# Kernel tuning notes

Measured on AMD Instinct MI355X. Metric: run time of the kernel, lower is better.

Reference implementation:

```python
import jax
import jax.numpy as jnp
import numpy as np

B, S, D, H, HID, E, TOPK = 1, 2048, 1024, 16, 4096, 8, 2
HEAD_DIM = D // H


def _layer_norm(x, g, b, eps=1e-5):
    mu = jnp.mean(x, axis=-1, keepdims=True)
    var = jnp.var(x, axis=-1, keepdims=True)
    return (x - mu) * jax.lax.rsqrt(var + eps) * g + b


def setup_inputs() -> dict:
    key = jax.random.key(0)
    ks = jax.random.split(key, 12)
    s = 0.02
    return {
        "x": jax.random.normal(ks[0], (B, S, D), jnp.float32),
        "ln1_g": jnp.ones((D,), jnp.float32),
        "ln1_b": jnp.zeros((D,), jnp.float32),
        "wq": jax.random.normal(ks[1], (D, D), jnp.float32) * s,
        "wk": jax.random.normal(ks[2], (D, D), jnp.float32) * s,
        "wv": jax.random.normal(ks[3], (D, D), jnp.float32) * s,
        "wo": jax.random.normal(ks[4], (D, D), jnp.float32) * s,
        "ln2_g": jnp.ones((D,), jnp.float32),
        "ln2_b": jnp.zeros((D,), jnp.float32),
        "w_gate": jax.random.normal(ks[5], (D, E), jnp.float32) * s,
        "w_eg": jax.random.normal(ks[6], (E, D, HID), jnp.float32) * s,
        "w_eu": jax.random.normal(ks[7], (E, D, HID), jnp.float32) * s,
        "w_ed": jax.random.normal(ks[8], (E, HID, D), jnp.float32) * s,
    }


def _attention(h, wq, wk, wv, wo):
    b, s, d = h.shape
    q = (h @ wq).reshape(b, s, H, HEAD_DIM).transpose(0, 2, 1, 3)
    k = (h @ wk).reshape(b, s, H, HEAD_DIM).transpose(0, 2, 1, 3)
    v = (h @ wv).reshape(b, s, H, HEAD_DIM).transpose(0, 2, 1, 3)
    scores = jnp.einsum("bhqd,bhkd->bhqk", q, k) / jnp.sqrt(jnp.asarray(HEAD_DIM, h.dtype))
    causal = jnp.tril(jnp.ones((s, s), bool))  # [s,s]
    scores = jnp.where(causal, scores, jnp.asarray(-1e30, h.dtype))
    attn = jax.nn.softmax(scores, axis=-1)
    out = jnp.einsum("bhqk,bhkd->bhqd", attn, v).transpose(0, 2, 1, 3).reshape(b, s, d)
    return out @ wo


def _moe(h, w_gate, w_eg, w_eu, w_ed):
    b, s, d = h.shape
    flat = h.reshape(-1, d)  # [T,D]
    logits = flat @ w_gate  # [T,E]
    scores = jax.nn.sigmoid(logits)
    top_val, top_idx = jax.lax.top_k(scores, TOPK)
    top_val = top_val / (jnp.sum(top_val, axis=-1, keepdims=True) + 1e-9)
    # per-token per-expert combine weight (0 for unrouted experts)
    combine = jnp.sum(jax.nn.one_hot(top_idx, E, dtype=flat.dtype) * top_val[..., None], axis=1)  # [T,E]
    g = jax.nn.silu(jnp.einsum("td,edh->eth", flat, w_eg))
    u = jnp.einsum("td,edh->eth", flat, w_eu)
    eo = jnp.einsum("eth,ehd->etd", g * u, w_ed)  # [E,T,D]
    out = jnp.einsum("etd,te->td", eo, combine)
    return out.reshape(b, s, d)


def reference(x, ln1_g, ln1_b, wq, wk, wv, wo, ln2_g, ln2_b, w_gate, w_eg, w_eu, w_ed):
    x = x + _attention(_layer_norm(x, ln1_g, ln1_b), wq, wk, wv, wo)
    x = x + _moe(_layer_norm(x, ln2_g, ln2_b), w_gate, w_eg, w_eu, w_ed)
    return x
```

## Files before the change

### kernel.cpp

```cpp
#include <hip/hip_runtime.h>
#include <hip/hip_bf16.h>
#include <stdint.h>

#define DI __device__ __forceinline__

typedef short bf16x8_t __attribute__((ext_vector_type(8)));
typedef float f32x4_t __attribute__((ext_vector_type(4)));

DI unsigned short f2bf(float f) {
  __hip_bfloat16 h = __float2bfloat16(f);
  unsigned short u;
  __builtin_memcpy(&u, &h, 2);
  return u;
}

DI uint32_t pk2(float a, float b) {
  return (uint32_t)f2bf(a) | ((uint32_t)f2bf(b) << 16);
}

DI f32x4_t mfma16(bf16x8_t a, bf16x8_t b, f32x4_t c) {
  return __builtin_amdgcn_mfma_f32_16x16x32_bf16(a, b, c, 0, 0, 0);
}

DI void gload16(const void* g, void* l) {
  __builtin_amdgcn_global_load_lds(
      (const __attribute__((address_space(1))) uint32_t*)g,
      (__attribute__((address_space(3))) uint32_t*)l, 16, 0, 0);
}

DI bf16x8_t frag(const unsigned short* base, int row, int hi) {
  return *(const bf16x8_t*)&base[row * 32 + ((hi ^ ((row >> 1) & 3)) * 8)];
}
DI int chunk_swz(int tid) { return ((tid & 3) ^ ((tid >> 3) & 3)) * 8; }

__global__ __launch_bounds__(256) void transpose_cvt(const float* __restrict__ in,
                                                     unsigned short* __restrict__ out,
                                                     int R, int C) {
  __shared__ float tile[64][65];
  const int tid = threadIdx.x;
  const int tx = tid & 15, ty = tid >> 4;
  const size_t zoff = (size_t)blockIdx.z * R * C;
  const int r0 = blockIdx.y * 64, c0 = blockIdx.x * 64;
#pragma unroll
  for (int i = 0; i < 4; ++i) {
    const int r = ty + i * 16;
    const float4 v = *(const float4*)(in + zoff + (size_t)(r0 + r) * C + c0 + tx * 4);
    tile[r][tx * 4 + 0] = v.x; tile[r][tx * 4 + 1] = v.y;
    tile[r][tx * 4 + 2] = v.z; tile[r][tx * 4 + 3] = v.w;
  }
  __syncthreads();
#pragma unroll
  for (int i = 0; i < 4; ++i) {
    const int r = ty + i * 16;
    ushort4 o;
    o.x = f2bf(tile[tx * 4 + 0][r]); o.y = f2bf(tile[tx * 4 + 1][r]);
    o.z = f2bf(tile[tx * 4 + 2][r]); o.w = f2bf(tile[tx * 4 + 3][r]);
    *(ushort4*)(out + zoff + (size_t)(c0 + r) * R + r0 + tx * 4) = o;
  }
}

__global__ __launch_bounds__(256) void ln_kernel(const float* __restrict__ x, const float* __restrict__ g,
                                                 const float* __restrict__ b, unsigned short* __restrict__ out) {
  const int row = blockIdx.x, tid = threadIdx.x;
  const int wid = tid >> 6, lane = tid & 63;
  const float4 v = *(const float4*)(x + (size_t)row * 1024 + tid * 4);
  float s = v.x + v.y + v.z + v.w;
  float s2 = v.x * v.x + v.y * v.y + v.z * v.z + v.w * v.w;
#pragma unroll
  for (int o = 1; o < 64; o <<= 1) { s += __shfl_xor(s, o); s2 += __shfl_xor(s2, o); }
  __shared__ float red[8];
  if (lane == 0) { red[wid] = s; red[4 + wid] = s2; }
  __syncthreads();
  const float ts = red[0] + red[1] + red[2] + red[3];
  const float ts2 = red[4] + red[5] + red[6] + red[7];
  const float mu = ts * 0.0009765625f;
  const float var = ts2 * 0.0009765625f - mu * mu;
  const float rs = rsqrtf(var + 1e-5f);
  const float4 gg = *(const float4*)(g + tid * 4);
  const float4 bb = *(const float4*)(b + tid * 4);
  ushort4 o4;
  o4.x = f2bf((v.x - mu) * rs * gg.x + bb.x);
  o4.y = f2bf((v.y - mu) * rs * gg.y + bb.y);
  o4.z = f2bf((v.z - mu) * rs * gg.z + bb.z);
  o4.w = f2bf((v.w - mu) * rs * gg.w + bb.w);
  *(ushort4*)(out + (size_t)row * 1024 + tid * 4) = o4;
}

template<int BN>
DI void gemm_loop(const unsigned short* aR0, const unsigned short* aR1,
                  const unsigned short* bR0, const unsigned short* bR1,
                  const int K, unsigned short* lds, const int tid,
                  f32x4_t (&acc)[4][BN / 32]) {
  constexpr int NF = BN / 32;
  unsigned short* ldsA = lds;
  unsigned short* ldsB = lds + 4096;
  const int wid = tid >> 6, lane = tid & 63, ln = lane & 15, hi = lane >> 4;
  const int wr = wid >> 1, wc = wid & 1;
  char* dstA0 = (char*)ldsA + wid * 1024;
  char* dstA1 = (char*)ldsA + 4096 + wid * 1024;
  char* dstB0 = (char*)ldsB + wid * 1024;
  char* dstB1 = (char*)ldsB + 4096 + wid * 1024;
  for (int k0 = 0; k0 < K; k0 += 32) {
    gload16(aR0 + k0, dstA0);
    gload16(aR1 + k0, dstA1);
    gload16(bR0 + k0, dstB0);
    if constexpr (BN == 128) gload16(bR1 + k0, dstB1);
    __syncthreads();
    bf16x8_t af[4];
#pragma unroll
    for (int mf = 0; mf < 4; ++mf)
      af[mf] = frag(ldsA, wr * 64 + mf * 16 + ln, hi);
#pragma unroll
    for (int nf = 0; nf < NF; ++nf) {
      bf16x8_t bfr = frag(ldsB, wc * (BN / 2) + nf * 16 + ln, hi);
#pragma unroll
      for (int mf = 0; mf < 4; ++mf)
        acc[mf][nf] = mfma16(af[mf], bfr, acc[mf][nf]);
    }
    __syncthreads();
  }
}

__global__ __launch_bounds__(256) void qkv_kernel(const unsigned short* __restrict__ h1,
                                                  const unsigned short* __restrict__ wqT,
                                                  const unsigned short* __restrict__ wkT,
                                                  const unsigned short* __restrict__ wvT,
                                                  unsigned short* __restrict__ qb,
                                                  unsigned short* __restrict__ kbf,
                                                  unsigned short* __restrict__ vt) {
  __shared__ unsigned short lds[128 * 32 + 128 * 32];
  const int tid = threadIdx.x;
  const int z = blockIdx.z;
  const unsigned short* BT = (z == 0) ? wqT : (z == 1) ? wkT : wvT;
  const int m0 = blockIdx.y * 128, n0 = blockIdx.x * 128;
  f32x4_t acc[4][4] = {};
  const int cs = chunk_swz(tid);
  const unsigned short* aR0 = h1 + (size_t)(m0 + (tid >> 2)) * 1024 + cs;
  const unsigned short* aR1 = aR0 + 64 * 1024;
  const unsigned short* bR0 = BT + (size_t)(n0 + (tid >> 2)) * 1024 + cs;
  const unsigned short* bR1 = bR0 + 64 * 1024;
  gemm_loop<128>(aR0, aR1, bR0, bR1, 1024, lds, tid, acc);
  const int lane = tid & 63, ln = lane & 15, hi = lane >> 4, wid = tid >> 6;
  const int wr = wid >> 1, wc = wid & 1;
  if (z < 2) {
    unsigned short* o = z ? kbf : qb;
#pragma unroll
    for (int mf = 0; mf < 4; ++mf)
#pragma unroll
      for (int nf = 0; nf < 4; ++nf)
#pragma unroll
        for (int r = 0; r < 4; ++r) {
          const int m = m0 + wr * 64 + mf * 16 + hi * 4 + r;
          const int n = n0 + wc * 64 + nf * 16 + ln;
          o[(size_t)m * 1024 + n] = f2bf(acc[mf][nf][r]);
        }
  } else {
#pragma unroll
    for (int mf = 0; mf < 4; ++mf)
#pragma unroll
      for (int nf = 0; nf < 4; ++nf) {
        const int n = n0 + wc * 64 + nf * 16 + ln;
        const int mb = m0 + wr * 64 + mf * 16 + hi * 4;
        ushort4 o;
        o.x = f2bf(acc[mf][nf][0]); o.y = f2bf(acc[mf][nf][1]);
        o.z = f2bf(acc[mf][nf][2]); o.w = f2bf(acc[mf][nf][3]);
        *(ushort4*)(vt + (size_t)n * 2048 + mb) = o;
      }
  }
}

__global__ __launch_bounds__(256) void wo_kernel(const unsigned short* __restrict__ ao,
                                                 const unsigned short* __restrict__ woT,
                                                 const float* __restrict__ x,
                                                 float* __restrict__ out) {
  __shared__ unsigned short lds[128 * 32 + 64 * 32];
  const int tid = threadIdx.x;
  const int m0 = blockIdx.y * 128, n0 = blockIdx.x * 64;
  f32x4_t acc[4][2] = {};
  const int cs = chunk_swz(tid);
  const unsigned short* aR0 = ao + (size_t)(m0 + (tid >> 2)) * 1024 + cs;
  const unsigned short* aR1 = aR0 + 64 * 1024;
  const unsigned short* bR0 = woT + (size_t)(n0 + (tid >> 2)) * 1024 + cs;
  gemm_loop<64>(aR0, aR1, bR0, nullptr, 1024, lds, tid, acc);
  const int lane = tid & 63, ln = lane & 15, hi = lane >> 4, wid = tid >> 6;
  const int wr = wid >> 1, wc = wid & 1;
#pragma unroll
  for (int mf = 0; mf < 4; ++mf)
#pragma unroll
    for (int nf = 0; nf < 2; ++nf)
#pragma unroll
      for (int r = 0; r < 4; ++r) {
        const int m = m0 + wr * 64 + mf * 16 + hi * 4 + r;
        const int n = n0 + wc * 32 + nf * 16 + ln;
        out[(size_t)m * 1024 + n] = acc[mf][nf][r] + x[(size_t)m * 1024 + n];
      }
}

__global__ __launch_bounds__(256) void attn_kernel(const unsigned short* __restrict__ qb,
                                                   const unsigned short* __restrict__ kbuf,
                                                   const unsigned short* __restrict__ vt,
                                                   unsigned short* __restrict__ ao) {
  __shared__ unsigned short kTl[4096];
  __shared__ unsigned short vTl[4096];
  __shared__ unsigned short pl[4][1024];
  const int tid = threadIdx.x;
  const int wid = tid >> 6, lane = tid & 63;
  const int ln = lane & 15, hi = lane >> 4;
  const int h = blockIdx.y;
  const int q0 = blockIdx.x * 64;
  const int q0w = q0 + wid * 16;

  const unsigned short* qrow = qb + (size_t)(q0w + ln) * 1024 + h * 64 + hi * 8;
  const bf16x8_t aq0 = *(const bf16x8_t*)(qrow);
  const bf16x8_t aq1 = *(const bf16x8_t*)(qrow + 32);

  const int str_r = tid >> 3, str_c = tid & 7;
  const int swc = (str_c ^ (str_r & 7)) * 8;
  const unsigned short* ksrc0 = kbuf + (size_t)str_r * 1024 + h * 64 + swc;
  const unsigned short* ksrc1 = kbuf + (size_t)(str_r + 32) * 1024 + h * 64 + swc;
  const unsigned short* vsrc0 = vt + (size_t)(h * 64 + str_r) * 2048 + swc;
  const unsigned short* vsrc1 = vt + (size_t)(h * 64 + str_r + 32) * 2048 + swc;
  char* kd0 = (char*)kTl + wid * 1024;
  char* kd1 = (char*)kTl + 4096 + wid * 1024;
  char* vd0 = (char*)vTl + wid * 1024;
  char* vd1 = (char*)vTl + 4096 + wid * 1024;

  float m_r[4], l_r[4];
  f32x4_t o_acc[4] = {};
#pragma unroll
  for (int r = 0; r < 4; ++r) { m_r[r] = -1e30f; l_r[r] = 0.f; }

  const int nkv = blockIdx.x + 1;
  for (int it = 0; it < nkv; ++it) {
    const int kv0 = it * 64;
    gload16(ksrc0 + (size_t)kv0 * 1024, kd0);
    gload16(ksrc1 + (size_t)kv0 * 1024, kd1);
    gload16(vsrc0 + kv0, vd0);
    gload16(vsrc1 + kv0, vd1);
    __syncthreads();

    float sc[4][4];
#pragma unroll
    for (int cf = 0; cf < 4; ++cf) {
      const int row = cf * 16 + ln;
      const int swz = row & 7;
      const bf16x8_t b0 = *(const bf16x8_t*)((char*)kTl + row * 128 + ((hi ^ swz) * 16));
      const bf16x8_t b1 = *(const bf16x8_t*)((char*)kTl + row * 128 + (((4 + hi) ^ swz) * 16));
      f32x4_t zacc = {};
      zacc = mfma16(aq0, b0, zacc);
      zacc = mfma16(aq1, b1, zacc);
#pragma unroll
      for (int r = 0; r < 4; ++r) sc[cf][r] = zacc[r] * 0.125f;
    }
    if (kv0 + 63 > q0w) {
#pragma unroll
      for (int cf = 0; cf < 4; ++cf)
#pragma unroll
        for (int r = 0; r < 4; ++r) {
          const int qg = q0w + hi * 4 + r;
          const int kg = kv0 + cf * 16 + ln;
          if (kg > qg) sc[cf][r] = -1e30f;
        }
    }
#pragma unroll
    for (int r = 0; r < 4; ++r) {
      float tm = fmaxf(fmaxf(sc[0][r], sc[1][r]), fmaxf(sc[2][r], sc[3][r]));
      tm = fmaxf(tm, __shfl_xor(tm, 1));
      tm = fmaxf(tm, __shfl_xor(tm, 2));
      tm = fmaxf(tm, __shfl_xor(tm, 4));
      tm = fmaxf(tm, __shfl_xor(tm, 8));
      const float mn = fmaxf(m_r[r], tm);
      const float alpha = __expf(m_r[r] - mn);
      float rsum = 0.f;
#pragma unroll
      for (int cf = 0; cf < 4; ++cf) {
        const float p = __expf(sc[cf][r] - mn);
        sc[cf][r] = p; rsum += p;
      }
      rsum += __shfl_xor(rsum, 1); rsum += __shfl_xor(rsum, 2);
      rsum += __shfl_xor(rsum, 4); rsum += __shfl_xor(rsum, 8);
      l_r[r] = l_r[r] * alpha + rsum;
      m_r[r] = mn;
#pragma unroll
      for (int df = 0; df < 4; ++df) o_acc[df][r] *= alpha;
    }
    unsigned short* pw = &pl[wid][0];
#pragma unroll
    for (int cf = 0; cf < 4; ++cf)
#pragma unroll
      for (int r = 0; r < 4; ++r) {
        const int qq = hi * 4 + r;
        const int kv = cf * 16 + ln;
        const int bo = (qq * 128 + kv * 2) ^ ((qq & 7) << 4);
        *(unsigned short*)((char*)pw + bo) = f2bf(sc[cf][r]);
      }
    __syncthreads();
    const bf16x8_t pa0 = *(const bf16x8_t*)((char*)pw + ((ln * 128 + hi * 16) ^ ((ln & 7) << 4)));
    const bf16x8_t pa1 = *(const bf16x8_t*)((char*)pw + ((ln * 128 + 64 + hi * 16) ^ ((ln & 7) << 4)));
#pragma unroll
    for (int df = 0; df < 4; ++df) {
      const int d = df * 16 + ln;
      const int swz = d & 7;
      const bf16x8_t bv0 = *(const bf16x8_t*)((char*)vTl + d * 128 + ((hi ^ swz) * 16));
      const bf16x8_t bv1 = *(const bf16x8_t*)((char*)vTl + d * 128 + (((4 + hi) ^ swz) * 16));
      o_acc[df] = mfma16(pa0, bv0, o_acc[df]);
      o_acc[df] = mfma16(pa1, bv1, o_acc[df]);
    }
    __syncthreads();
  }
#pragma unroll
  for (int df = 0; df < 4; ++df) {
    const int n = h * 64 + df * 16 + ln;
#pragma unroll
    for (int r = 0; r < 4; ++r) {
      const int m = q0w + hi * 4 + r;
      ao[(size_t)m * 1024 + n] = f2bf(o_acc[df][r] / l_r[r]);
    }
  }
}

__global__ __launch_bounds__(256) void gate_kernel(const float* __restrict__ x2, const float* __restrict__ g,
                                                   const float* __restrict__ b, const float* __restrict__ wg,
                                                   int2* __restrict__ te, float2* __restrict__ tw,
                                                   int* __restrict__ cnt) {
  const int tid = threadIdx.x, wid = tid >> 6, lane = tid & 63;
  const int t = blockIdx.x * 4 + wid;
  const float* row = x2 + (size_t)t * 1024;
  float vv[16];
#pragma unroll
  for (int i = 0; i < 4; ++i) *(float4*)&vv[i * 4] = *(const float4*)(row + lane * 16 + i * 4);
  float s = 0.f, s2 = 0.f;
#pragma unroll
  for (int j = 0; j < 16; ++j) { s += vv[j]; s2 += vv[j] * vv[j]; }
#pragma unroll
  for (int o = 1; o < 64; o <<= 1) { s += __shfl_xor(s, o); s2 += __shfl_xor(s2, o); }
  const float mu = s * 0.0009765625f;
  const float var = s2 * 0.0009765625f - mu * mu;
  const float rs = rsqrtf(var + 1e-5f);
  float acc[8] = {0.f, 0.f, 0.f, 0.f, 0.f, 0.f, 0.f, 0.f};
#pragma unroll
  for (int j = 0; j < 16; ++j) {
    const int d = lane * 16 + j;
    const float xv = (vv[j] - mu) * rs * g[d] + b[d];
    const float4 w0 = *(const float4*)(wg + d * 8);
    const float4 w1 = *(const float4*)(wg + d * 8 + 4);
    acc[0] += xv * w0.x; acc[1] += xv * w0.y; acc[2] += xv * w0.z; acc[3] += xv * w0.w;
    acc[4] += xv * w1.x; acc[5] += xv * w1.y; acc[6] += xv * w1.z; acc[7] += xv * w1.w;
  }
#pragma unroll
  for (int o = 1; o < 64; o <<= 1) {
#pragma unroll
    for (int e = 0; e < 8; ++e) acc[e] += __shfl_xor(acc[e], o);
  }
  if (lane == 0) {
    float sg[8];
#pragma unroll
    for (int e = 0; e < 8; ++e) sg[e] = 1.f / (1.f + __expf(-acc[e]));
    int e0 = 0;
#pragma unroll
    for (int e = 1; e < 8; ++e) if (sg[e] > sg[e0]) e0 = e;
    int e1 = (e0 == 0) ? 1 : 0;
#pragma unroll
    for (int e = 0; e < 8; ++e) if (e != e0 && sg[e] > sg[e1]) e1 = e;
    const float v0 = sg[e0], v1 = sg[e1];
    const float inv = 1.f / (v0 + v1 + 1e-9f);
    te[t] = make_int2(e0, e1);
    tw[t] = make_float2(v0 * inv, v1 * inv);
    atomicAdd(&cnt[e0], 1);
    atomicAdd(&cnt[e1], 1);
  }
}

__global__ void zero_counters(int* p) { if (threadIdx.x < 8) p[threadIdx.x] = 0; }

__global__ __launch_bounds__(256) void g2_kernel(const int* __restrict__ cnt, int* __restrict__ slot_off,
                                                 int* __restrict__ tile_expert, int* __restrict__ tile_rowbase,
                                                 int* __restrict__ cursor, int* __restrict__ assign_token,
                                                 float* __restrict__ assign_w) {
  const int tid = threadIdx.x;
  for (int i = tid; i < 8192; i += 256) { assign_token[i] = -1; assign_w[i] = 0.f; }
  if (tid == 0) {
    int base = 0, tiles = 0;
    for (int e = 0; e < 8; ++e) {
      const int c = cnt[e];
      slot_off[e] = base;
      cursor[e] = 0;
      const int nt = (c + 255) >> 8;
      for (int i = 0; i < nt; ++i) {
        tile_expert[tiles] = e;
        tile_rowbase[tiles] = base + i * 256;
        ++tiles;
      }
      base += nt * 256;
    }
    for (; tiles < 40; ++tiles) tile_expert[tiles] = -1;
  }
}

__global__ __launch_bounds__(256) void g3_kernel(const int2* __restrict__ te, const float2* __restrict__ tw,
                                                 const int* __restrict__ slot_off, int* __restrict__ cursor,
                                                 int* __restrict__ assign_token, float* __restrict__ assign_w) {
  const int t = blockIdx.x * 256 + threadIdx.x;
  const int2 e = te[t];
  const float2 w = tw[t];
  const int s0 = slot_off[e.x] + atomicAdd(&cursor[e.x], 1);
  assign_token[s0] = t; assign_w[s0] = w.x;
  const int s1 = slot_off[e.y] + atomicAdd(&cursor[e.y], 1);
  assign_token[s1] = t; assign_w[s1] = w.y;
}

DI void stageA4(const unsigned short* a0, const unsigned short* a1,
                const unsigned short* a2, const unsigned short* a3,
                int koff, char* Ab, int wid) {
  gload16(a0 + koff, Ab + wid * 1024);
  gload16(a1 + koff, Ab + 4096 + wid * 1024);
  gload16(a2 + koff, Ab + 8192 + wid * 1024);
  gload16(a3 + koff, Ab + 12288 + wid * 1024);
}
DI void stageA2(const unsigned short* a0, const unsigned short* a1,
                int koff, char* Ab, int wid) {
  gload16(a0 + koff, Ab + wid * 1024);
  gload16(a1 + koff, Ab + 4096 + wid * 1024);
}

DI void ug_write_b(char* Bn, const int* boff, const float4& q0, const float4& q1,
                   const float4& q2, const float4& q3) {
  const float* q0p = (const float*)&q0; const float* q1p = (const float*)&q1;
  const float* q2p = (const float*)&q2; const float* q3p = (const float*)&q3;
#pragma unroll
  for (int i = 0; i < 4; ++i) {
    uint2 w;
    w.x = pk2(q0p[i], q1p[i]);
    w.y = pk2(q2p[i], q3p[i]);
    *(uint2*)(Bn + boff[i]) = w;
  }
}

DI void ug_mfma256(const unsigned short* A, const char* Bb, int wr, int wc, int ln, int hi,
                   f32x4_t (&accg)[8][2], f32x4_t (&accu)[8][2]) {
  bf16x8_t af[8];
#pragma unroll
  for (int mf = 0; mf < 8; ++mf)
    af[mf] = frag(A, wr * 128 + mf * 16 + ln, hi);
#pragma unroll
  for (int nf = 0; nf < 2; ++nf) {
    const int nrow = wc * 32 + nf * 16 + ln;
    int bo = nrow * 64 + hi * 16;
    bo ^= ((nrow >> 2) & 7) << 4;
    const bf16x8_t bg = *(const bf16x8_t*)(Bb + bo);
    const bf16x8_t bu = *(const bf16x8_t*)(Bb + 4096 + bo);
#pragma unroll
    for (int mf = 0; mf < 8; ++mf) {
      accg[mf][nf] = mfma16(af[mf], bg, accg[mf][nf]);
      accu[mf][nf] = mfma16(af[mf], bu, accu[mf][nf]);
    }
  }
}

__global__ __launch_bounds__(256, 2) void upgate_kernel(const unsigned short* __restrict__ h2,
                                                        const float* __restrict__ w_eg, const float* __restrict__ w_eu,
                                                        const int* __restrict__ tile_expert,
                                                        const int* __restrict__ tile_rowbase,
                                                        const int* __restrict__ assign_token,
                                                        unsigned short* __restrict__ act) {
  const int by = blockIdx.y;
  const int e = tile_expert[by];
  if (e < 0) return;
  const int n0 = blockIdx.x * 64;
  const int rowbase = tile_rowbase[by];
  const int tid = threadIdx.x;
  __shared__ unsigned short lds[2 * 8192 + 2 * 4096];
  char* A0 = (char*)lds;
  char* A1 = (char*)lds + 16384;
  char* B0 = (char*)lds + 32768;
  char* B1 = (char*)lds + 40960;
  const int wid = tid >> 6, lane = tid & 63, ln = lane & 15, hi = lane >> 4;
  const int wr = wid >> 1, wc = wid & 1;
  const int r0s = rowbase + (tid >> 2);
  int tk0 = assign_token[r0s];        tk0 = tk0 < 0 ? 0 : tk0;
  int tk1 = assign_token[r0s + 64];   tk1 = tk1 < 0 ? 0 : tk1;
  int tk2 = assign_token[r0s + 128];  tk2 = tk2 < 0 ? 0 : tk2;
  int tk3 = assign_token[r0s + 192];  tk3 = tk3 < 0 ? 0 : tk3;
  const int cs = chunk_swz(tid);
  const unsigned short* aR0 = h2 + (size_t)tk0 * 1024 + cs;
  const unsigned short* aR1 = h2 + (size_t)tk1 * 1024 + cs;
  const unsigned short* aR2 = h2 + (size_t)tk2 * 1024 + cs;
  const unsigned short* aR3 = h2 + (size_t)tk3 * 1024 + cs;
  const int mat = tid >> 7;
  const int blk = tid & 127;
  const int kb = (blk >> 4) * 4;
  const int nb = (blk & 15) * 4;
  const float* bsrc = (mat ? w_eu : w_eg) + (size_t)e * 1024 * 4096 + (size_t)kb * 4096 + n0 + nb;
  int boff[4];
#pragma unroll
  for (int i = 0; i < 4; ++i) {
    const int n = nb + i;
    int bo = mat * 4096 + n * 64 + kb * 2;
    bo ^= ((n >> 2) & 7) << 4;
    boff[i] = bo;
  }
  f32x4_t accg[8][2] = {};
  f32x4_t accu[8][2] = {};
  float4 qA0, qA1, qA2, qA3, qB0, qB1, qB2, qB3;
  stageA4(aR0, aR1, aR2, aR3, 0, A0, wid);
  qB0 = *(const float4*)(bsrc);
  qB1 = *(const float4*)(bsrc + 4096);
  qB2 = *(const float4*)(bsrc + 8192);
  qB3 = *(const float4*)(bsrc + 12288);
  __builtin_amdgcn_sched_barrier(0);
  ug_write_b(B0, boff, qB0, qB1, qB2, qB3);
  {
    const float* bs = bsrc + (size_t)32 * 4096;
    qA0 = *(const float4*)(bs);
    qA1 = *(const float4*)(bs + 4096);
    qA2 = *(const float4*)(bs + 8192);
    qA3 = *(const float4*)(bs + 12288);
  }
  asm volatile("s_waitcnt lgkmcnt(0)" ::: "memory");
  __builtin_amdgcn_sched_barrier(0);
  __builtin_amdgcn_s_barrier();
  for (int p = 0; p < 15; ++p) {
    {
      const int t = 2 * p;
      stageA4(aR0, aR1, aR2, aR3, (t + 1) * 32, A1, wid);
      const float* bs = bsrc + (size_t)(t + 2) * 32 * 4096;
      qB0 = *(const float4*)(bs);
      qB1 = *(const float4*)(bs + 4096);
      qB2 = *(const float4*)(bs + 8192);
      qB3 = *(const float4*)(bs + 12288);
      __builtin_amdgcn_sched_barrier(0);
      ug_write_b(B1, boff, qA0, qA1, qA2, qA3);
      ug_mfma256((const unsigned short*)A0, B0, wr, wc, ln, hi, accg, accu);
      asm volatile("s_waitcnt vmcnt(4)" ::: "memory");
      __builtin_amdgcn_sched_barrier(0);
      asm volatile("s_waitcnt lgkmcnt(0)" ::: "memory");
      __builtin_amdgcn_sched_barrier(0);
      __builtin_amdgcn_s_barrier();
    }
    {
      const int t = 2 * p + 1;
      stageA4(aR0, aR1, aR2, aR3, (t + 1) * 32, A0, wid);
      const float* bs = bsrc + (size_t)(t + 2) * 32 * 4096;
      qA0 = *(const float4*)(bs);
      qA1 = *(const float4*)(bs + 4096);
      qA2 = *(const float4*)(bs + 8192);
      qA3 = *(const float4*)(bs + 12288);
      __builtin_amdgcn_sched_barrier(0);
      ug_write_b(B0, boff, qB0, qB1, qB2, qB3);
      ug_mfma256((const unsigned short*)A1, B1, wr, wc, ln, hi, accg, accu);
      asm volatile("s_waitcnt vmcnt(4)" ::: "memory");
      __builtin_amdgcn_sched_barrier(0);
      asm volatile("s_waitcnt lgkmcnt(0)" ::: "memory");
      __builtin_amdgcn_sched_barrier(0);
      __builtin_amdgcn_s_barrier();
    }
  }
  stageA4(aR0, aR1, aR2, aR3, 31 * 32, A1, wid);
  __builtin_amdgcn_sched_barrier(0);
  ug_write_b(B1, boff, qA0, qA1, qA2, qA3);
  ug_mfma256((const unsigned short*)A0, B0, wr, wc, ln, hi, accg, accu);
  asm volatile("s_waitcnt vmcnt(0)" ::: "memory");
  __builtin_amdgcn_sched_barrier(0);
  asm volatile("s_waitcnt lgkmcnt(0)" ::: "memory");
  __builtin_amdgcn_sched_barrier(0);
  __builtin_amdgcn_s_barrier();
  ug_mfma256((const unsigned short*)A1, B1, wr, wc, ln, hi, accg, accu);
#pragma unroll
  for (int mf = 0; mf < 8; ++mf)
#pragma unroll
    for (int nf = 0; nf < 2; ++nf)
#pragma unroll
      for (int r = 0; r < 4; ++r) {
        const int m = wr * 128 + mf * 16 + hi * 4 + r;
        const int n = n0 + wc * 32 + nf * 16 + ln;
        const float gv = accg[mf][nf][r], uv = accu[mf][nf][r];
        const float val = gv / (1.f + __expf(-gv)) * uv;
        act[(size_t)(rowbase + m) * 4096 + n] = f2bf(val);
      }
}

DI void dn_write_b(char* Bn, const int* boff, const float4& q0, const float4& q1) {
  const float* q0p = (const float*)&q0; const float* q1p = (const float*)&q1;
#pragma unroll
  for (int i = 0; i < 4; ++i)
    *(uint32_t*)(Bn + boff[i]) = pk2(q0p[i], q1p[i]);
}

DI void dn_mfma(const unsigned short* A, const char* Bb, int wr, int wc, int ln, int hi,
                f32x4_t (&acc)[4][2]) {
  bf16x8_t af[4];
#pragma unroll
  for (int mf = 0; mf < 4; ++mf)
    af[mf] = frag(A, wr * 64 + mf * 16 + ln, hi);
#pragma unroll
  for (int nf = 0; nf < 2; ++nf) {
    const int nrow = wc * 32 + nf * 16 + ln;
    int bo = nrow * 64 + hi * 16;
    bo ^= ((nrow >> 2) & 7) << 4;
    const bf16x8_t bb = *(const bf16x8_t*)(Bb + bo);
#pragma unroll
    for (int mf = 0; mf < 4; ++mf)
      acc[mf][nf] = mfma16(af[mf], bb, acc[mf][nf]);
  }
}

__global__ __launch_bounds__(256) void down_kernel(const unsigned short* __restrict__ act,
                                                   const float* __restrict__ w_ed,
                                                   const int* __restrict__ tile_expert,
                                                   const int* __restrict__ tile_rowbase,
                                                   const int* __restrict__ assign_token,
                                                   const float* __restrict__ assign_w,
                                                   float* __restrict__ out) {
  const int tix = blockIdx.y;
  const int e = tile_expert[tix >> 1];
  if (e < 0) return;
  const int rowbase = tile_rowbase[tix >> 1] + (tix & 1) * 128;
  const int n0 = blockIdx.x * 64;
  const int kz = blockIdx.z * 1024;
  const int tid = threadIdx.x;
  __shared__ unsigned short lds[2 * 4096 + 2 * 2048];
  char* A0 = (char*)lds;
  char* A1 = (char*)lds + 8192;
  char* B0 = (char*)lds + 16384;
  char* B1 = (char*)lds + 20480;
  const int wid = tid >> 6, lane = tid & 63, ln = lane & 15, hi = lane >> 4;
  const int wr = wid >> 1, wc = wid & 1;
  const int cs = chunk_swz(tid);
  const unsigned short* aR0 = act + (size_t)(rowbase + (tid >> 2)) * 4096 + kz + cs;
  const unsigned short* aR1 = aR0 + (size_t)64 * 4096;
  const int nb = (tid & 15) * 4;
  const int kb2 = (tid >> 4) * 2;
  const float* bsrc = w_ed + (size_t)e * 4096 * 1024 + (size_t)(kz + kb2) * 1024 + n0 + nb;
  int boff[4];
#pragma unroll
  for (int i = 0; i < 4; ++i) {
    const int n = nb + i;
    int bo = n * 64 + kb2 * 2;
    bo ^= ((n >> 2) & 7) << 4;
    boff[i] = bo;
  }
  f32x4_t acc[4][2] = {};
  float4 qA0, qA1, qB0, qB1;
  stageA2(aR0, aR1, 0, A0, wid);
  qB0 = *(const float4*)(bsrc);
  qB1 = *(const float4*)(bsrc + 1024);
  __builtin_amdgcn_sched_barrier(0);
  dn_write_b(B0, boff, qB0, qB1);
  {
    const float* bs = bsrc + (size_t)32 * 1024;
    qA0 = *(const float4*)(bs);
    qA1 = *(const float4*)(bs + 1024);
  }
  asm volatile("s_waitcnt lgkmcnt(0)" ::: "memory");
  __builtin_amdgcn_sched_barrier(0);
  __builtin_amdgcn_s_barrier();
  for (int p = 0; p < 15; ++p) {
    {
      const int t = 2 * p;
      stageA2(aR0, aR1, (t + 1) * 32, A1, wid);
      const float* bs = bsrc + (size_t)(t + 2) * 32 * 1024;
      qB0 = *(const float4*)(bs);
      qB1 = *(const float4*)(bs + 1024);
      __builtin_amdgcn_sched_barrier(0);
      dn_write_b(B1, boff, qA0, qA1);
      dn_mfma((const unsigned short*)A0, B0, wr, wc, ln, hi, acc);
      asm volatile("s_waitcnt vmcnt(2)" ::: "memory");
      __builtin_amdgcn_sched_barrier(0);
      asm volatile("s_waitcnt lgkmcnt(0)" ::: "memory");
      __builtin_amdgcn_sched_barrier(0);
      __builtin_amdgcn_s_barrier();
    }
    {
      const int t = 2 * p + 1;
      stageA2(aR0, aR1, (t + 1) * 32, A0, wid);
      const float* bs = bsrc + (size_t)(t + 2) * 32 * 1024;
      qA0 = *(const float4*)(bs);
      qA1 = *(const float4*)(bs + 1024);
      __builtin_amdgcn_sched_barrier(0);
      dn_write_b(B0, boff, qB0, qB1);
      dn_mfma((const unsigned short*)A1, B1, wr, wc, ln, hi, acc);
      asm volatile("s_waitcnt vmcnt(2)" ::: "memory");
      __builtin_amdgcn_sched_barrier(0);
      asm volatile("s_waitcnt lgkmcnt(0)" ::: "memory");
      __builtin_amdgcn_sched_barrier(0);
      __builtin_amdgcn_s_barrier();
    }
  }
  stageA2(aR0, aR1, 31 * 32, A1, wid);
  __builtin_amdgcn_sched_barrier(0);
  dn_write_b(B1, boff, qA0, qA1);
  dn_mfma((const unsigned short*)A0, B0, wr, wc, ln, hi, acc);
  asm volatile("s_waitcnt vmcnt(0)" ::: "memory");
  __builtin_amdgcn_sched_barrier(0);
  asm volatile("s_waitcnt lgkmcnt(0)" ::: "memory");
  __builtin_amdgcn_sched_barrier(0);
  __builtin_amdgcn_s_barrier();
  dn_mfma((const unsigned short*)A1, B1, wr, wc, ln, hi, acc);
#pragma unroll
  for (int mf = 0; mf < 4; ++mf)
#pragma unroll
    for (int r = 0; r < 4; ++r) {
      const int m = wr * 64 + mf * 16 + hi * 4 + r;
      const int slot = rowbase + m;
      const int tk = assign_token[slot];
      if (tk >= 0) {
        const float w = assign_w[slot];
#pragma unroll
        for (int nf = 0; nf < 2; ++nf) {
          const int n = n0 + wc * 32 + nf * 16 + ln;
          atomicAdd(out + (size_t)tk * 1024 + n, acc[mf][nf][r] * w);
        }
      }
    }
}

extern "C" void kernel_launch(void* const* d_in, const int* in_sizes, int n_in,
                              void* d_out, int out_size, void* d_ws, size_t ws_size,
                              hipStream_t stream) {
  (void)in_sizes; (void)n_in; (void)out_size;
  const float* x    = (const float*)d_in[0];
  const float* ln1g = (const float*)d_in[1];
  const float* ln1b = (const float*)d_in[2];
  const float* wq   = (const float*)d_in[3];
  const float* wk   = (const float*)d_in[4];
  const float* wv   = (const float*)d_in[5];
  const float* wo   = (const float*)d_in[6];
  const float* ln2g = (const float*)d_in[7];
  const float* ln2b = (const float*)d_in[8];
  const float* wg   = (const float*)d_in[9];
  const float* weg  = (const float*)d_in[10];
  const float* weu  = (const float*)d_in[11];
  const float* wed  = (const float*)d_in[12];
  float* out = (float*)d_out;
  char* ws = (char*)d_ws;

  const size_t MB = (size_t)1 << 20;
  if (ws_size < 86 * MB) return;
  unsigned short* wqT = (unsigned short*)(ws + 0 * MB);
  unsigned short* wkT = (unsigned short*)(ws + 2 * MB);
  unsigned short* wvT = (unsigned short*)(ws + 4 * MB);
  unsigned short* woT = (unsigned short*)(ws + 6 * MB);
  unsigned short* h1  = (unsigned short*)(ws + 8 * MB);
  unsigned short* qb  = (unsigned short*)(ws + 12 * MB);
  unsigned short* kbf = (unsigned short*)(ws + 16 * MB);
  unsigned short* vt  = (unsigned short*)(ws + 20 * MB);
  unsigned short* ao  = (unsigned short*)(ws + 24 * MB);
  unsigned short* h2  = (unsigned short*)(ws + 28 * MB);
  unsigned short* act = (unsigned short*)(ws + 32 * MB);
  int2*   te = (int2*)(ws + 84 * MB);
  float2* tw = (float2*)(ws + 84 * MB + 16384);
  int*  meta = (int*)(ws + 84 * MB + 32768);
  int* cnt = meta;
  int* cursor = meta + 8;
  int* slot_off = meta + 16;
  int* tile_expert = meta + 24;
  int* tile_rowbase = meta + 64;
  int*   assign_token = (int*)(ws + 84 * MB + 36864);
  float* assign_w     = (float*)(ws + 84 * MB + 36864 + 32768);

  zero_counters<<<1, 64, 0, stream>>>(cnt);
  transpose_cvt<<<dim3(16, 16, 1), 256, 0, stream>>>(wq, wqT, 1024, 1024);
  transpose_cvt<<<dim3(16, 16, 1), 256, 0, stream>>>(wk, wkT, 1024, 1024);
  transpose_cvt<<<dim3(16, 16, 1), 256, 0, stream>>>(wv, wvT, 1024, 1024);
  transpose_cvt<<<dim3(16, 16, 1), 256, 0, stream>>>(wo, woT, 1024, 1024);
  ln_kernel<<<2048, 256, 0, stream>>>(x, ln1g, ln1b, h1);
  qkv_kernel<<<dim3(8, 16, 3), 256, 0, stream>>>(h1, wqT, wkT, wvT, qb, kbf, vt);
  attn_kernel<<<dim3(32, 16), 256, 0, stream>>>(qb, kbf, vt, ao);
  wo_kernel<<<dim3(16, 16), 256, 0, stream>>>(ao, woT, x, out);
  ln_kernel<<<2048, 256, 0, stream>>>(out, ln2g, ln2b, h2);
  gate_kernel<<<512, 256, 0, stream>>>(out, ln2g, ln2b, wg, te, tw, cnt);
  g2_kernel<<<1, 256, 0, stream>>>(cnt, slot_off, tile_expert, tile_rowbase, cursor, assign_token, assign_w);
  g3_kernel<<<8, 256, 0, stream>>>(te, tw, slot_off, cursor, assign_token, assign_w);
  upgate_kernel<<<dim3(64, 24), 256, 0, stream>>>(h2, weg, weu, tile_expert, tile_rowbase, assign_token, act);
  down_kernel<<<dim3(16, 48, 4), 256, 0, stream>>>(act, wed, tile_expert, tile_rowbase, assign_token, assign_w, out);
}
```

Measured before the change: 495.7 us.

## Triple-buffer A tiles in MoE up/gate and down GEMM kernels

Switches the A-operand LDS staging in both MoE expert GEMM kernels from double to triple buffering, prefetching A two k-steps ahead with relaxed vmcnt waits. This gives the gathered token-row loads more time in flight before they are consumed, to hide global memory latency. It grows LDS use (the up/gate kernel goes from 48KB to 64KB per block), which may limit the two-blocks-per-CU occupancy target, and the loop becomes a six-step rotation.

```diff
diff --git a/kernel.cpp b/kernel.cpp
--- a/kernel.cpp
+++ b/kernel.cpp
@@ -469,11 +469,12 @@
   const int n0 = blockIdx.x * 64;
   const int rowbase = tile_rowbase[by];
   const int tid = threadIdx.x;
-  __shared__ unsigned short lds[2 * 8192 + 2 * 4096];
-  char* A0 = (char*)lds;
-  char* A1 = (char*)lds + 16384;
-  char* B0 = (char*)lds + 32768;
-  char* B1 = (char*)lds + 40960;
+  __shared__ unsigned short lds[3 * 8192 + 2 * 4096];
+  char* Ab0 = (char*)lds;
+  char* Ab1 = (char*)lds + 16384;
+  char* Ab2 = (char*)lds + 32768;
+  char* BL0 = (char*)lds + 49152;
+  char* BL1 = (char*)lds + 57344;
   const int wid = tid >> 6, lane = tid & 63, ln = lane & 15, hi = lane >> 4;
   const int wr = wid >> 1, wc = wid & 1;
   const int r0s = rowbase + (tid >> 2);
@@ -502,13 +503,16 @@
   f32x4_t accg[8][2] = {};
   f32x4_t accu[8][2] = {};
   float4 qA0, qA1, qA2, qA3, qB0, qB1, qB2, qB3;
-  stageA4(aR0, aR1, aR2, aR3, 0, A0, wid);
+  stageA4(aR0, aR1, aR2, aR3, 0, Ab0, wid);
   qB0 = *(const float4*)(bsrc);
   qB1 = *(const float4*)(bsrc + 4096);
   qB2 = *(const float4*)(bsrc + 8192);
   qB3 = *(const float4*)(bsrc + 12288);
-  __builtin_amdgcn_sched_barrier(0);
-  ug_write_b(B0, boff, qB0, qB1, qB2, qB3);
+  stageA4(aR0, aR1, aR2, aR3, 32, Ab1, wid);
+  __builtin_amdgcn_sched_barrier(0);
+  asm volatile("s_waitcnt vmcnt(4)" ::: "memory");
+  __builtin_amdgcn_sched_barrier(0);
+  ug_write_b(BL0, boff, qB0, qB1, qB2, qB3);
   {
     const float* bs = bsrc + (size_t)32 * 4096;
     qA0 = *(const float4*)(bs);
@@ -519,52 +523,41 @@
   asm volatile("s_waitcnt lgkmcnt(0)" ::: "memory");
   __builtin_amdgcn_sched_barrier(0);
   __builtin_amdgcn_s_barrier();
-  for (int p = 0; p < 15; ++p) {
-    {
-      const int t = 2 * p;
-      stageA4(aR0, aR1, aR2, aR3, (t + 1) * 32, A1, wid);
-      const float* bs = bsrc + (size_t)(t + 2) * 32 * 4096;
-      qB0 = *(const float4*)(bs);
-      qB1 = *(const float4*)(bs + 4096);
-      qB2 = *(const float4*)(bs + 8192);
-      qB3 = *(const float4*)(bs + 12288);
-      __builtin_amdgcn_sched_barrier(0);
-      ug_write_b(B1, boff, qA0, qA1, qA2, qA3);
-      ug_mfma256((const unsigned short*)A0, B0, wr, wc, ln, hi, accg, accu);
-      asm volatile("s_waitcnt vmcnt(4)" ::: "memory");
-      __builtin_amdgcn_sched_barrier(0);
-      asm volatile("s_waitcnt lgkmcnt(0)" ::: "memory");
-      __builtin_amdgcn_sched_barrier(0);
-      __builtin_amdgcn_s_barrier();
-    }
-    {
-      const int t = 2 * p + 1;
-      stageA4(aR0, aR1, aR2, aR3, (t + 1) * 32, A0, wid);
-      const float* bs = bsrc + (size_t)(t + 2) * 32 * 4096;
-      qA0 = *(const float4*)(bs);
-      qA1 = *(const float4*)(bs + 4096);
-      qA2 = *(const float4*)(bs + 8192);
-      qA3 = *(const float4*)(bs + 12288);
-      __builtin_amdgcn_sched_barrier(0);
-      ug_write_b(B0, boff, qB0, qB1, qB2, qB3);
-      ug_mfma256((const unsigned short*)A1, B1, wr, wc, ln, hi, accg, accu);
-      asm volatile("s_waitcnt vmcnt(4)" ::: "memory");
-      __builtin_amdgcn_sched_barrier(0);
-      asm volatile("s_waitcnt lgkmcnt(0)" ::: "memory");
-      __builtin_amdgcn_sched_barrier(0);
-      __builtin_amdgcn_s_barrier();
-    }
-  }
-  stageA4(aR0, aR1, aR2, aR3, 31 * 32, A1, wid);
-  __builtin_amdgcn_sched_barrier(0);
-  ug_write_b(B1, boff, qA0, qA1, qA2, qA3);
-  ug_mfma256((const unsigned short*)A0, B0, wr, wc, ln, hi, accg, accu);
+#define UG_STEP(T, ACUR, APF, BCUR, BNXT, QWR0, QWR1, QWR2, QWR3, QLD0, QLD1, QLD2, QLD3)   \
+  {                                                                                         \
+    stageA4(aR0, aR1, aR2, aR3, ((T) + 2) * 32, APF, wid);                                  \
+    const float* bs_ = bsrc + (size_t)((T) + 2) * 32 * 4096;                                \
+    QLD0 = *(const float4*)(bs_);                                                           \
+    QLD1 = *(const float4*)(bs_ + 4096);                                                    \
+    QLD2 = *(const float4*)(bs_ + 8192);                                                    \
+    QLD3 = *(const float4*)(bs_ + 12288);                                                   \
+    __builtin_amdgcn_sched_barrier(0);                                                      \
+    asm volatile("s_waitcnt vmcnt(8)" ::: "memory");                                        \
+    __builtin_amdgcn_sched_barrier(0);                                                      \
+    ug_write_b(BNXT, boff, QWR0, QWR1, QWR2, QWR3);                                         \
+    ug_mfma256((const unsigned short*)(ACUR), BCUR, wr, wc, ln, hi, accg, accu);            \
+    asm volatile("s_waitcnt lgkmcnt(0)" ::: "memory");                                      \
+    __builtin_amdgcn_sched_barrier(0);                                                      \
+    __builtin_amdgcn_s_barrier();                                                           \
+  }
+  for (int p = 0; p < 5; ++p) {
+    const int t = p * 6;
+    UG_STEP(t + 0, Ab0, Ab2, BL0, BL1, qA0, qA1, qA2, qA3, qB0, qB1, qB2, qB3);
+    UG_STEP(t + 1, Ab1, Ab0, BL1, BL0, qB0, qB1, qB2, qB3, qA0, qA1, qA2, qA3);
+    UG_STEP(t + 2, Ab2, Ab1, BL0, BL1, qA0, qA1, qA2, qA3, qB0, qB1, qB2, qB3);
+    UG_STEP(t + 3, Ab0, Ab2, BL1, BL0, qB0, qB1, qB2, qB3, qA0, qA1, qA2, qA3);
+    UG_STEP(t + 4, Ab1, Ab0, BL0, BL1, qA0, qA1, qA2, qA3, qB0, qB1, qB2, qB3);
+    UG_STEP(t + 5, Ab2, Ab1, BL1, BL0, qB0, qB1, qB2, qB3, qA0, qA1, qA2, qA3);
+  }
+#undef UG_STEP
   asm volatile("s_waitcnt vmcnt(0)" ::: "memory");
   __builtin_amdgcn_sched_barrier(0);
+  ug_write_b(BL1, boff, qA0, qA1, qA2, qA3);
+  ug_mfma256((const unsigned short*)Ab0, BL0, wr, wc, ln, hi, accg, accu);
   asm volatile("s_waitcnt lgkmcnt(0)" ::: "memory");
   __builtin_amdgcn_sched_barrier(0);
   __builtin_amdgcn_s_barrier();
-  ug_mfma256((const unsigned short*)A1, B1, wr, wc, ln, hi, accg, accu);
+  ug_mfma256((const unsigned short*)Ab1, BL1, wr, wc, ln, hi, accg, accu);
 #pragma unroll
   for (int mf = 0; mf < 8; ++mf)
 #pragma unroll
@@ -618,11 +611,12 @@
   const int n0 = blockIdx.x * 64;
   const int kz = blockIdx.z * 1024;
   const int tid = threadIdx.x;
-  __shared__ unsigned short lds[2 * 4096 + 2 * 2048];
-  char* A0 = (char*)lds;
-  char* A1 = (char*)lds + 8192;
-  char* B0 = (char*)lds + 16384;
-  char* B1 = (char*)lds + 20480;
+  __shared__ unsigned short lds[3 * 4096 + 2 * 2048];
+  char* Ab0 = (char*)lds;
+  char* Ab1 = (char*)lds + 8192;
+  char* Ab2 = (char*)lds + 16384;
+  char* BL0 = (char*)lds + 24576;
+  char* BL1 = (char*)lds + 28672;
   const int wid = tid >> 6, lane = tid & 63, ln = lane & 15, hi = lane >> 4;
   const int wr = wid >> 1, wc = wid & 1;
   const int cs = chunk_swz(tid);
@@ -641,11 +635,14 @@
   }
   f32x4_t acc[4][2] = {};
   float4 qA0, qA1, qB0, qB1;
-  stageA2(aR0, aR1, 0, A0, wid);
+  stageA2(aR0, aR1, 0, Ab0, wid);
   qB0 = *(const float4*)(bsrc);
   qB1 = *(const float4*)(bsrc + 1024);
-  __builtin_amdgcn_sched_barrier(0);
-  dn_write_b(B0, boff, qB0, qB1);
+  stageA2(aR0, aR1, 32, Ab1, wid);
+  __builtin_amdgcn_sched_barrier(0);
+  asm volatile("s_waitcnt vmcnt(2)" ::: "memory");
+  __builtin_amdgcn_sched_barrier(0);
+  dn_write_b(BL0, boff, qB0, qB1);
   {
     const float* bs = bsrc + (size_t)32 * 1024;
     qA0 = *(const float4*)(bs);
@@ -654,48 +651,39 @@
   asm volatile("s_waitcnt lgkmcnt(0)" ::: "memory");
   __builtin_amdgcn_sched_barrier(0);
   __builtin_amdgcn_s_barrier();
-  for (int p = 0; p < 15; ++p) {
-    {
-      const int t = 2 * p;
-      stageA2(aR0, aR1, (t + 1) * 32, A1, wid);
-      const float* bs = bsrc + (size_t)(t + 2) * 32 * 1024;
-      qB0 = *(const float4*)(bs);
-      qB1 = *(const float4*)(bs + 1024);
-      __builtin_amdgcn_sched_barrier(0);
-      dn_write_b(B1, boff, qA0, qA1);
-      dn_mfma((const unsigned short*)A0, B0, wr, wc, ln, hi, acc);
-      asm volatile("s_waitcnt vmcnt(2)" ::: "memory");
-      __builtin_amdgcn_sched_barrier(0);
-      asm volatile("s_waitcnt lgkmcnt(0)" ::: "memory");
-      __builtin_amdgcn_sched_barrier(0);
-      __builtin_amdgcn_s_barrier();
-    }
-    {
-      const int t = 2 * p + 1;
-      stageA2(aR0, aR1, (t + 1) * 32, A0, wid);
-      const float* bs = bsrc + (size_t)(t + 2) * 32 * 1024;
-      qA0 = *(const float4*)(bs);
-      qA1 = *(const float4*)(bs + 1024);
-      __builtin_amdgcn_sched_barrier(0);
-      dn_write_b(B0, boff, qB0, qB1);
-      dn_mfma((const unsigned short*)A1, B1, wr, wc, ln, hi, acc);
-      asm volatile("s_waitcnt vmcnt(2)" ::: "memory");
-      __builtin_amdgcn_sched_barrier(0);
-      asm volatile("s_waitcnt lgkmcnt(0)" ::: "memory");
-      __builtin_amdgcn_sched_barrier(0);
-      __builtin_amdgcn_s_barrier();
-    }
-  }
-  stageA2(aR0, aR1, 31 * 32, A1, wid);
-  __builtin_amdgcn_sched_barrier(0);
-  dn_write_b(B1, boff, qA0, qA1);
-  dn_mfma((const unsigned short*)A0, B0, wr, wc, ln, hi, acc);
+#define DN_STEP(T, ACUR, APF, BCUR, BNXT, QWR0, QWR1, QLD0, QLD1)                           \
+  {                                                                                         \
+    stageA2(aR0, aR1, ((T) + 2) * 32, APF, wid);                                            \
+    const float* bs_ = bsrc + (size_t)((T) + 2) * 32 * 1024;                                \
+    QLD0 = *(const float4*)(bs_);                                                           \
+    QLD1 = *(const float4*)(bs_ + 1024);                                                    \
+    __builtin_amdgcn_sched_barrier(0);                                                      \
+    asm volatile("s_waitcnt vmcnt(4)" ::: "memory");                                        \
+    __builtin_amdgcn_sched_barrier(0);                                                      \
+    dn_write_b(BNXT, boff, QWR0, QWR1);                                                     \
+    dn_mfma((const unsigned short*)(ACUR), BCUR, wr, wc, ln, hi, acc);                      \
+    asm volatile("s_waitcnt lgkmcnt(0)" ::: "memory");                                      \
+    __builtin_amdgcn_sched_barrier(0);                                                      \
+    __builtin_amdgcn_s_barrier();                                                           \
+  }
+  for (int p = 0; p < 5; ++p) {
+    const int t = p * 6;
+    DN_STEP(t + 0, Ab0, Ab2, BL0, BL1, qA0, qA1, qB0, qB1);
+    DN_STEP(t + 1, Ab1, Ab0, BL1, BL0, qB0, qB1, qA0, qA1);
+    DN_STEP(t + 2, Ab2, Ab1, BL0, BL1, qA0, qA1, qB0, qB1);
+    DN_STEP(t + 3, Ab0, Ab2, BL1, BL0, qB0, qB1, qA0, qA1);
+    DN_STEP(t + 4, Ab1, Ab0, BL0, BL1, qA0, qA1, qB0, qB1);
+    DN_STEP(t + 5, Ab2, Ab1, BL1, BL0, qB0, qB1, qA0, qA1);
+  }
+#undef DN_STEP
   asm volatile("s_waitcnt vmcnt(0)" ::: "memory");
   __builtin_amdgcn_sched_barrier(0);
+  dn_write_b(BL1, boff, qA0, qA1);
+  dn_mfma((const unsigned short*)Ab0, BL0, wr, wc, ln, hi, acc);
   asm volatile("s_waitcnt lgkmcnt(0)" ::: "memory");
   __builtin_amdgcn_sched_barrier(0);
   __builtin_amdgcn_s_barrier();
-  dn_mfma((const unsigned short*)A1, B1, wr, wc, ln, hi, acc);
+  dn_mfma((const unsigned short*)Ab1, BL1, wr, wc, ln, hi, acc);
 #pragma unroll
   for (int mf = 0; mf < 4; ++mf)
 #pragma unroll
```

Measured after the change: 502.8 us. About the same (+1.4%).
